# Performance work log

Measured on AMD Instinct MI355X. Metric: run time of the kernel, lower is better.

Reference implementation:

```python
import jax, jax.numpy as jnp
import numpy as np

B, N, E, H = 16, 1024, 1024, 16
D = E // H  # head size = 64

def setup_inputs() -> dict:
    key = jax.random.key(0)
    ks = jax.random.split(key, 5)
    s = 1.0 / np.sqrt(E)
    return {
        "x": jax.random.normal(ks[0], (B, N, E), dtype=jnp.float32),
        "W_qkv": jax.random.normal(ks[1], (E, 3 * E), dtype=jnp.float32) * s,
        "b_qkv": jnp.zeros((3 * E,), dtype=jnp.float32),
        "W_proj": jax.random.normal(ks[2], (E, E), dtype=jnp.float32) * s,
        "b_proj": jnp.zeros((E,), dtype=jnp.float32),
    }

def reference(x, W_qkv, b_qkv, W_proj, b_proj):
    # qkv projection: [B,N,3E]
    qkv = x @ W_qkv + b_qkv
    q, k, v = jnp.split(qkv, 3, axis=-1)
    # b n (h d) -> b h n d
    def split_heads(t):
        return t.reshape(B, N, H, D).transpose(0, 2, 1, 3)
    q, k, v = split_heads(q), split_heads(k), split_heads(v)
    scale = D ** -0.5
    attn = jnp.einsum('bhnd,bhmd->bhnm', q, k) * scale  # [B,H,N,N]
    attn = jax.nn.softmax(attn, axis=-1)
    # dropout p=0 -> identity
    o = jnp.einsum('bhnm,bhmd->bhnd', attn, v)  # [B,H,N,D]
    o = o.transpose(0, 2, 1, 3).reshape(B, N, E)  # b h n d -> b n (h d)
    return o @ W_proj + b_proj
```

## Files before the change

kernel.cpp:

```cpp
#include <hip/hip_runtime.h>
#include <hip/hip_bf16.h>
#include <math.h>

#define BB 16
#define NN 1024
#define EE 1024
#define HH 16
#define DD 64
#define THREE_E 3072
#define M_TOTAL (BB * NN)

typedef __attribute__((ext_vector_type(8))) short bf16x8;
typedef __attribute__((ext_vector_type(4))) short bf16x4;
typedef __attribute__((ext_vector_type(4))) float floatx4;

#define SCALE_Q 0.18033688011112042f

static __device__ __forceinline__ unsigned short f2bf(float f) {
    union { float f; unsigned u; } x; x.f = f;
    unsigned r = x.u + 0x7fffu + ((x.u >> 16) & 1u);
    return (unsigned short)(r >> 16);
}

static __device__ __forceinline__ float fast_exp2(float x) {
#if __has_builtin(__builtin_amdgcn_exp2f)
    return __builtin_amdgcn_exp2f(x);
#else
    float r; __asm__("v_exp_f32 %0, %1" : "=v"(r) : "v"(x)); return r;
#endif
}

static __device__ __forceinline__ bf16x8 pack8v(floatx4 a, floatx4 b) {
    union { bf16x8 v; unsigned u[4]; } r;
    __hip_bfloat162 t;
    t = __float22bfloat162_rn(make_float2(a[0], a[1])); r.u[0] = *(unsigned*)&t;
    t = __float22bfloat162_rn(make_float2(a[2], a[3])); r.u[1] = *(unsigned*)&t;
    t = __float22bfloat162_rn(make_float2(b[0], b[1])); r.u[2] = *(unsigned*)&t;
    t = __float22bfloat162_rn(make_float2(b[2], b[3])); r.u[3] = *(unsigned*)&t;
    return r.v;
}
static __device__ __forceinline__ bf16x8 pack8f(float4 a, float4 b) {
    union { bf16x8 v; unsigned u[4]; } r;
    __hip_bfloat162 t;
    t = __float22bfloat162_rn(make_float2(a.x, a.y)); r.u[0] = *(unsigned*)&t;
    t = __float22bfloat162_rn(make_float2(a.z, a.w)); r.u[1] = *(unsigned*)&t;
    t = __float22bfloat162_rn(make_float2(b.x, b.y)); r.u[2] = *(unsigned*)&t;
    t = __float22bfloat162_rn(make_float2(b.z, b.w)); r.u[3] = *(unsigned*)&t;
    return r.v;
}

#define ASYNC16(gp, lp)                                                \
    __builtin_amdgcn_global_load_lds(                                  \
        (const __attribute__((address_space(1))) void*)(gp),           \
        (__attribute__((address_space(3))) void*)(lp), 16, 0, 0)

#define DRAIN_VMEM() __asm__ __volatile__("s_waitcnt vmcnt(0)" ::: "memory")

__global__ __launch_bounds__(256) void convert_x(
    const float* __restrict__ x, unsigned short* __restrict__ xb)
{
    int i = blockIdx.x * 256 + threadIdx.x;
    const float4* xp = (const float4*)x;
    float4 a = xp[i * 2], b = xp[i * 2 + 1];
    *(bf16x8*)&xb[i * 8] = pack8f(a, b);
}

__global__ __launch_bounds__(256) void wtrans(
    const float* __restrict__ w, unsigned short* __restrict__ wt, int R, int C)
{
    __shared__ float tile[32][33];
    const int t = threadIdx.x;
    const int lr = t >> 5, lc = t & 31;
    const int r0 = blockIdx.y * 32, c0 = blockIdx.x * 32;
    #pragma unroll
    for (int p = 0; p < 4; ++p)
        tile[lr + p * 8][lc] = w[(size_t)(r0 + lr + p * 8) * C + c0 + lc];
    __syncthreads();
    #pragma unroll
    for (int p = 0; p < 4; ++p) {
        int oc = lr + p * 8;
        float v = tile[lc][oc];
        wt[(size_t)(c0 + oc) * R + r0 + lc] = f2bf(v);
    }
}

__global__ __launch_bounds__(256) void gemm_qkv_mfma(
    const unsigned short* __restrict__ xb,
    const unsigned short* __restrict__ wt,
    const float* __restrict__ bias,
    unsigned short* __restrict__ Qo, unsigned short* __restrict__ Ko,
    unsigned short* __restrict__ Vo)
{
    __shared__ __align__(16) unsigned short As[128 * 64];
    __shared__ __align__(16) unsigned short Bs[128 * 64];

    const int t = threadIdx.x;
    const int w = t >> 6, lane = t & 63;
    const int quad = lane >> 4, l15 = lane & 15;
    const int wm = w >> 1, wn = w & 1;
    const int m0 = blockIdx.y * 128;
    const int n0 = blockIdx.x * 128;
    const int srow = lane >> 3;
    const int sch  = lane & 7;
    const int scw  = (sch ^ srow) * 8;
    const int rb   = l15 & 7;

    floatx4 acc[4][4];
    #pragma unroll
    for (int i = 0; i < 4; ++i)
        #pragma unroll
        for (int j = 0; j < 4; ++j) acc[i][j] = (floatx4){0.f, 0.f, 0.f, 0.f};

    const unsigned short* aG = &xb[(size_t)(m0 + w * 8 + srow) * EE + scw];
    const unsigned short* bG = &wt[(size_t)(n0 + w * 8 + srow) * EE + scw];

    for (int kk = 0; kk < EE; kk += 64) {
        #pragma unroll
        for (int p = 0; p < 4; ++p) {
            ASYNC16(aG + kk + (size_t)(p * 32) * EE, &As[(w * 8 + p * 32) * 64]);
            ASYNC16(bG + kk + (size_t)(p * 32) * EE, &Bs[(w * 8 + p * 32) * 64]);
        }
        DRAIN_VMEM();
        __syncthreads();

        #pragma unroll
        for (int s = 0; s < 2; ++s) {
            const int rsw = (((s << 2) | quad) ^ rb) * 8;
            bf16x8 af[4], bf[4];
            #pragma unroll
            for (int i = 0; i < 4; ++i) {
                af[i] = *(const bf16x8*)&As[(wm * 64 + i * 16 + l15) * 64 + rsw];
                bf[i] = *(const bf16x8*)&Bs[(wn * 64 + i * 16 + l15) * 64 + rsw];
            }
            #pragma unroll
            for (int i = 0; i < 4; ++i)
                #pragma unroll
                for (int j = 0; j < 4; ++j)
                    acc[i][j] = __builtin_amdgcn_mfma_f32_16x16x32_bf16(
                        af[i], bf[j], acc[i][j], 0, 0, 0);
        }
        __syncthreads();
    }

    const int mb = m0 + wm * 64;
    const int nb = n0 + wn * 64;
    #pragma unroll
    for (int i = 0; i < 4; ++i) {
        #pragma unroll
        for (int j = 0; j < 4; ++j) {
            int nc = nb + j * 16;
            int which = nc >> 10;
            int e0 = nc & 1023;
            int h  = e0 >> 6;
            int d0 = e0 & 63;
            float bv = bias[nc + l15];
            #pragma unroll
            for (int r = 0; r < 4; ++r) {
                int m = mb + i * 16 + quad * 4 + r;
                int b = m >> 10, n = m & 1023;
                size_t off = ((size_t)(b * HH + h) * NN + n) * DD + d0 + l15;
                float v = acc[i][j][r] + bv;
                if (which == 0)      Qo[off] = f2bf(v * SCALE_Q);
                else if (which == 1) Ko[off] = f2bf(v);
                else                 Vo[off] = f2bf(v);
            }
        }
    }
}

__global__ __launch_bounds__(256) void vtrans(
    const unsigned short* __restrict__ V, unsigned short* __restrict__ Vt)
{
    __shared__ __align__(16) unsigned short tile[64][72];
    const int t  = threadIdx.x;
    const int bh = blockIdx.x;
    const int n0 = blockIdx.y * 64;
    const int r  = t >> 2, c = t & 3;

    const unsigned short* src = &V[((size_t)bh * NN + n0 + r) * DD + c * 16];
    bf16x8 v0 = *(const bf16x8*)&src[0];
    bf16x8 v1 = *(const bf16x8*)&src[8];
    #pragma unroll
    for (int k = 0; k < 8; ++k) tile[c * 16 + k][r]     = v0[k];
    #pragma unroll
    for (int k = 0; k < 8; ++k) tile[c * 16 + 8 + k][r] = v1[k];
    __syncthreads();

    unsigned short* dst = &Vt[((size_t)bh * DD + r) * NN + n0 + c * 16];
    *(bf16x8*)&dst[0] = *(const bf16x8*)&tile[r][c * 16];
    *(bf16x8*)&dst[8] = *(const bf16x8*)&tile[r][c * 16 + 8];
}

__global__ __launch_bounds__(256) void attn_mfma(
    const unsigned short* __restrict__ Q,
    const unsigned short* __restrict__ K,
    const unsigned short* __restrict__ Vt,
    unsigned short* __restrict__ O)
{
    __shared__ __align__(16) unsigned short Ks[64 * 64];
    __shared__ __align__(16) unsigned short Vs[64 * 64];

    const int t    = threadIdx.x;
    const int w    = t >> 6;
    const int quad = (t >> 4) & 3;
    const int l15  = t & 15;
    const int i    = blockIdx.x;
    const int bh   = ((i >> 6) << 3) | (i & 7);
    const int qt   = (i >> 3) & 7;

    const unsigned short* Qg = Q  + (size_t)bh * NN * DD;
    const unsigned short* Kg = K  + (size_t)bh * NN * DD;
    const unsigned short* Vg = Vt + (size_t)bh * DD * NN;

    const int q0 = qt * 128 + w * 32;

    bf16x8 qf[2][2];
    #pragma unroll
    for (int a = 0; a < 2; ++a) {
        qf[a][0] = *(const bf16x8*)&Qg[(size_t)(q0 + a * 16 + l15) * DD + quad * 8];
        qf[a][1] = *(const bf16x8*)&Qg[(size_t)(q0 + a * 16 + l15) * DD + 32 + quad * 8];
    }

    bf16x8 onesA;
    #pragma unroll
    for (int z = 0; z < 8; ++z) onesA[z] = (short)0x3F80;

    floatx4 oa[2][4];
    #pragma unroll
    for (int a = 0; a < 2; ++a)
        #pragma unroll
        for (int jd = 0; jd < 4; ++jd) oa[a][jd] = (floatx4){0.f, 0.f, 0.f, 0.f};
    floatx4 ls[2];
    ls[0] = (floatx4){0.f, 0.f, 0.f, 0.f};
    ls[1] = (floatx4){0.f, 0.f, 0.f, 0.f};

    const int srow = t >> 2;
    const int sc   = t & 3;
    const int swz  = srow & 7;
    const int cbase = ((quad ^ (l15 & 7)) << 3);

    bf16x8 kr0, kr1, vr0, vr1;
    {
        const unsigned short* kg = &Kg[(size_t)srow * DD + sc * 16];
        kr0 = *(const bf16x8*)&kg[0];
        kr1 = *(const bf16x8*)&kg[8];
        const unsigned short* vg = &Vg[(size_t)srow * NN + sc * 16];
        vr0 = *(const bf16x8*)&vg[0];
        vr1 = *(const bf16x8*)&vg[8];
    }

    for (int kt = 0; kt < 16; ++kt) {
        __syncthreads();
        *(bf16x8*)&Ks[srow * 64 + (((2 * sc + 0) ^ swz) << 3)] = kr0;
        *(bf16x8*)&Ks[srow * 64 + (((2 * sc + 1) ^ swz) << 3)] = kr1;
        {
            bf16x4 h[4];
            h[0] = (bf16x4){vr0[0], vr0[1], vr0[2], vr0[3]};
            h[1] = (bf16x4){vr0[4], vr0[5], vr0[6], vr0[7]};
            h[2] = (bf16x4){vr1[0], vr1[1], vr1[2], vr1[3]};
            h[3] = (bf16x4){vr1[4], vr1[5], vr1[6], vr1[7]};
            #pragma unroll
            for (int q = 0; q < 4; ++q) {
                int col = ((((sc >> 1) * 4 + q) ^ swz) << 3) + ((sc & 1) << 2);
                *(bf16x4*)&Vs[srow * 64 + col] = h[q];
            }
        }
        __syncthreads();

        if (kt < 15) {
            const unsigned short* kg =
                &Kg[(size_t)((kt + 1) * 64 + srow) * DD + sc * 16];
            kr0 = *(const bf16x8*)&kg[0];
            kr1 = *(const bf16x8*)&kg[8];
            const unsigned short* vg =
                &Vg[(size_t)srow * NN + (kt + 1) * 64 + sc * 16];
            vr0 = *(const bf16x8*)&vg[0];
            vr1 = *(const bf16x8*)&vg[8];
        }

        floatx4 sa[2][4];
        #pragma unroll
        for (int a = 0; a < 2; ++a)
            #pragma unroll
            for (int tt = 0; tt < 4; ++tt) sa[a][tt] = (floatx4){0.f, 0.f, 0.f, 0.f};
        __builtin_amdgcn_s_setprio(1);
        #pragma unroll
        for (int tt = 0; tt < 4; ++tt) {
            const unsigned short* kb = &Ks[(tt * 16 + l15) * 64];
            bf16x8 kf0 = *(const bf16x8*)&kb[cbase];
            bf16x8 kf1 = *(const bf16x8*)&kb[cbase ^ 32];
            #pragma unroll
            for (int a = 0; a < 2; ++a) {
                sa[a][tt] = __builtin_amdgcn_mfma_f32_16x16x32_bf16(
                    kf0, qf[a][0], sa[a][tt], 0, 0, 0);
                sa[a][tt] = __builtin_amdgcn_mfma_f32_16x16x32_bf16(
                    kf1, qf[a][1], sa[a][tt], 0, 0, 0);
            }
        }
        __builtin_amdgcn_s_setprio(0);

        bf16x8 pf[2][2];
        #pragma unroll
        for (int a = 0; a < 2; ++a) {
            floatx4 pe[4];
            #pragma unroll
            for (int tt = 0; tt < 4; ++tt) {
                #pragma unroll
                for (int r = 0; r < 4; ++r)
                    pe[tt][r] = fast_exp2(sa[a][tt][r]);
            }
            pf[a][0] = pack8v(pe[0], pe[1]);
            pf[a][1] = pack8v(pe[2], pe[3]);
        }

        __builtin_amdgcn_s_setprio(1);
        #pragma unroll
        for (int a = 0; a < 2; ++a) {
            ls[a] = __builtin_amdgcn_mfma_f32_16x16x32_bf16(
                onesA, pf[a][0], ls[a], 0, 0, 0);
            ls[a] = __builtin_amdgcn_mfma_f32_16x16x32_bf16(
                onesA, pf[a][1], ls[a], 0, 0, 0);
        }
        #pragma unroll
        for (int jd = 0; jd < 4; ++jd) {
            const unsigned short* vb = &Vs[(jd * 16 + l15) * 64];
            bf16x8 vf0 = *(const bf16x8*)&vb[cbase];
            bf16x8 vf1 = *(const bf16x8*)&vb[cbase ^ 32];
            #pragma unroll
            for (int a = 0; a < 2; ++a) {
                oa[a][jd] = __builtin_amdgcn_mfma_f32_16x16x32_bf16(
                    vf0, pf[a][0], oa[a][jd], 0, 0, 0);
                oa[a][jd] = __builtin_amdgcn_mfma_f32_16x16x32_bf16(
                    vf1, pf[a][1], oa[a][jd], 0, 0, 0);
            }
        }
        __builtin_amdgcn_s_setprio(0);
    }

    const int b = bh >> 4, h = bh & 15;
    #pragma unroll
    for (int a = 0; a < 2; ++a) {
        float inv = 1.f / ls[a][0];
        int n = q0 + a * 16 + l15;
        size_t base = (size_t)(b * NN + n) * EE + h * DD;
        #pragma unroll
        for (int jd = 0; jd < 4; ++jd) {
            bf16x4 v;
            v[0] = (short)f2bf(oa[a][jd][0] * inv);
            v[1] = (short)f2bf(oa[a][jd][1] * inv);
            v[2] = (short)f2bf(oa[a][jd][2] * inv);
            v[3] = (short)f2bf(oa[a][jd][3] * inv);
            *(bf16x4*)&O[base + jd * 16 + quad * 4] = v;
        }
    }
}

__global__ __launch_bounds__(256) void gemm_proj_mfma(
    const unsigned short* __restrict__ Ob,
    const unsigned short* __restrict__ Bp,
    const float* __restrict__ bias, float* __restrict__ out)
{
    __shared__ __align__(16) unsigned short As[128 * 64];
    __shared__ __align__(16) unsigned short Bs[128 * 64];

    const int t = threadIdx.x;
    const int w = t >> 6, lane = t & 63;
    const int quad = lane >> 4, l15 = lane & 15;
    const int wm = w >> 1, wn = w & 1;
    const int m0 = blockIdx.y * 128;
    const int n0 = blockIdx.x * 128;
    const int srow = lane >> 3;
    const int sch  = lane & 7;
    const int scw  = (sch ^ srow) * 8;
    const int rb   = l15 & 7;

    floatx4 acc[4][4];
    #pragma unroll
    for (int i = 0; i < 4; ++i)
        #pragma unroll
        for (int j = 0; j < 4; ++j) acc[i][j] = (floatx4){0.f, 0.f, 0.f, 0.f};

    const unsigned short* aG = &Ob[(size_t)(m0 + w * 8 + srow) * EE + scw];
    const unsigned short* bG = &Bp[(size_t)(n0 + w * 8 + srow) * EE + scw];

    for (int kk = 0; kk < EE; kk += 64) {
        #pragma unroll
        for (int p = 0; p < 4; ++p) {
            ASYNC16(aG + kk + (size_t)(p * 32) * EE, &As[(w * 8 + p * 32) * 64]);
            ASYNC16(bG + kk + (size_t)(p * 32) * EE, &Bs[(w * 8 + p * 32) * 64]);
        }
        DRAIN_VMEM();
        __syncthreads();

        #pragma unroll
        for (int s = 0; s < 2; ++s) {
            const int rsw = (((s << 2) | quad) ^ rb) * 8;
            bf16x8 af[4], bf[4];
            #pragma unroll
            for (int i = 0; i < 4; ++i) {
                af[i] = *(const bf16x8*)&As[(wm * 64 + i * 16 + l15) * 64 + rsw];
                bf[i] = *(const bf16x8*)&Bs[(wn * 64 + i * 16 + l15) * 64 + rsw];
            }
            #pragma unroll
            for (int i = 0; i < 4; ++i)
                #pragma unroll
                for (int j = 0; j < 4; ++j)
                    acc[i][j] = __builtin_amdgcn_mfma_f32_16x16x32_bf16(
                        af[i], bf[j], acc[i][j], 0, 0, 0);
        }
        __syncthreads();
    }

    const int mb = m0 + wm * 64;
    const int nb = n0 + wn * 64;
    #pragma unroll
    for (int i = 0; i < 4; ++i) {
        #pragma unroll
        for (int j = 0; j < 4; ++j) {
            float bv = bias[nb + j * 16 + l15];
            #pragma unroll
            for (int r = 0; r < 4; ++r) {
                int mrow = mb + i * 16 + quad * 4 + r;
                out[(size_t)mrow * EE + nb + j * 16 + l15] = acc[i][j][r] + bv;
            }
        }
    }
}

extern "C" void kernel_launch(void* const* d_in, const int* in_sizes, int n_in,
                              void* d_out, int out_size, void* d_ws, size_t ws_size,
                              hipStream_t stream) {
    const float* x     = (const float*)d_in[0];
    const float* Wqkv  = (const float*)d_in[1];
    const float* bqkv  = (const float*)d_in[2];
    const float* Wproj = (const float*)d_in[3];
    const float* bproj = (const float*)d_in[4];
    float* out = (float*)d_out;

    const size_t BHND = (size_t)BB * HH * NN * DD;
    unsigned short* Q   = (unsigned short*)d_ws;
    unsigned short* K   = Q   + BHND;
    unsigned short* Vn  = K   + BHND;
    unsigned short* Vt  = Vn  + BHND;
    unsigned short* Ob  = Vt  + BHND;
    unsigned short* xb  = Ob  + BHND;
    unsigned short* Wqt = xb  + BHND;
    unsigned short* Wpt = Wqt + (size_t)THREE_E * EE;

    dim3 blk(256);
    convert_x<<<dim3(M_TOTAL * EE / (256 * 8)), blk, 0, stream>>>(x, xb);
    wtrans<<<dim3(THREE_E / 32, EE / 32), blk, 0, stream>>>(Wqkv, Wqt, EE, THREE_E);
    wtrans<<<dim3(EE / 32, EE / 32), blk, 0, stream>>>(Wproj, Wpt, EE, EE);

    gemm_qkv_mfma<<<dim3(THREE_E / 128, M_TOTAL / 128), blk, 0, stream>>>(
        xb, Wqt, bqkv, Q, K, Vn);
    vtrans<<<dim3(BB * HH, NN / 64), blk, 0, stream>>>(Vn, Vt);
    attn_mfma<<<dim3(BB * HH * NN / 128), blk, 0, stream>>>(Q, K, Vt, Ob);
    gemm_proj_mfma<<<dim3(EE / 128, M_TOTAL / 128), blk, 0, stream>>>(
        Ob, Wpt, bproj, out);
}
```

Before: 404.5 us.

## Double-buffer LDS tiles in QKV and projection GEMMs with async prefetch

Both GEMM kernels now keep two LDS buffers per operand. The tile for step k+1 is issued with global_load_lds while the MFMAs for step k run, which replaces the old load, drain, compute sequence that exposed memory latency on every step. MFMA sections are also wrapped in s_setprio to favour compute issue. This doubles LDS use to 64KB per block, which may lower occupancy. Correctness relies on the single barrier per iteration covering reuse of both buffers.

```diff
diff --git a/kernel.cpp b/kernel.cpp
--- a/kernel.cpp
+++ b/kernel.cpp
@@ -54,8 +54,6 @@
         (const __attribute__((address_space(1))) void*)(gp),           \
         (__attribute__((address_space(3))) void*)(lp), 16, 0, 0)
 
-#define DRAIN_VMEM() __asm__ __volatile__("s_waitcnt vmcnt(0)" ::: "memory")
-
 __global__ __launch_bounds__(256) void convert_x(
     const float* __restrict__ x, unsigned short* __restrict__ xb)
 {
@@ -91,8 +89,8 @@
     unsigned short* __restrict__ Qo, unsigned short* __restrict__ Ko,
     unsigned short* __restrict__ Vo)
 {
-    __shared__ __align__(16) unsigned short As[128 * 64];
-    __shared__ __align__(16) unsigned short Bs[128 * 64];
+    __shared__ __align__(16) unsigned short As[2][128 * 64];
+    __shared__ __align__(16) unsigned short Bs[2][128 * 64];
 
     const int t = threadIdx.x;
     const int w = t >> 6, lane = t & 63;
@@ -114,33 +112,47 @@
     const unsigned short* aG = &xb[(size_t)(m0 + w * 8 + srow) * EE + scw];
     const unsigned short* bG = &wt[(size_t)(n0 + w * 8 + srow) * EE + scw];
 
+#define STAGE_QKV(kk, sl) do {                                              \
+    _Pragma("unroll")                                                       \
+    for (int p = 0; p < 4; ++p) {                                           \
+        ASYNC16(aG + (kk) + (size_t)(p * 32) * EE,                          \
+                &As[sl][(w * 8 + p * 32) * 64]);                            \
+        ASYNC16(bG + (kk) + (size_t)(p * 32) * EE,                          \
+                &Bs[sl][(w * 8 + p * 32) * 64]);                            \
+    } } while (0)
+
+    STAGE_QKV(0, 0);
+    __asm__ __volatile__("s_waitcnt vmcnt(0)" ::: "memory");
+    __builtin_amdgcn_s_barrier();
+
+    #pragma unroll 1
     for (int kk = 0; kk < EE; kk += 64) {
-        #pragma unroll
-        for (int p = 0; p < 4; ++p) {
-            ASYNC16(aG + kk + (size_t)(p * 32) * EE, &As[(w * 8 + p * 32) * 64]);
-            ASYNC16(bG + kk + (size_t)(p * 32) * EE, &Bs[(w * 8 + p * 32) * 64]);
-        }
-        DRAIN_VMEM();
-        __syncthreads();
-
+        const int cur = (kk >> 6) & 1;
+        if (kk + 64 < EE) STAGE_QKV(kk + 64, cur ^ 1);
+        const unsigned short* Asl = As[cur];
+        const unsigned short* Bsl = Bs[cur];
         #pragma unroll
         for (int s = 0; s < 2; ++s) {
             const int rsw = (((s << 2) | quad) ^ rb) * 8;
-            bf16x8 af[4], bf[4];
+            bf16x8 af[4], bfv[4];
             #pragma unroll
             for (int i = 0; i < 4; ++i) {
-                af[i] = *(const bf16x8*)&As[(wm * 64 + i * 16 + l15) * 64 + rsw];
-                bf[i] = *(const bf16x8*)&Bs[(wn * 64 + i * 16 + l15) * 64 + rsw];
-            }
+                af[i]  = *(const bf16x8*)&Asl[(wm * 64 + i * 16 + l15) * 64 + rsw];
+                bfv[i] = *(const bf16x8*)&Bsl[(wn * 64 + i * 16 + l15) * 64 + rsw];
+            }
+            __builtin_amdgcn_s_setprio(1);
             #pragma unroll
             for (int i = 0; i < 4; ++i)
                 #pragma unroll
                 for (int j = 0; j < 4; ++j)
                     acc[i][j] = __builtin_amdgcn_mfma_f32_16x16x32_bf16(
-                        af[i], bf[j], acc[i][j], 0, 0, 0);
-        }
-        __syncthreads();
-    }
+                        af[i], bfv[j], acc[i][j], 0, 0, 0);
+            __builtin_amdgcn_s_setprio(0);
+        }
+        __asm__ __volatile__("s_waitcnt vmcnt(0)" ::: "memory");
+        __builtin_amdgcn_s_barrier();
+    }
+#undef STAGE_QKV
 
     const int mb = m0 + wm * 64;
     const int nb = n0 + wn * 64;
@@ -360,8 +372,8 @@
     const unsigned short* __restrict__ Bp,
     const float* __restrict__ bias, float* __restrict__ out)
 {
-    __shared__ __align__(16) unsigned short As[128 * 64];
-    __shared__ __align__(16) unsigned short Bs[128 * 64];
+    __shared__ __align__(16) unsigned short As[2][128 * 64];
+    __shared__ __align__(16) unsigned short Bs[2][128 * 64];
 
     const int t = threadIdx.x;
     const int w = t >> 6, lane = t & 63;
@@ -383,33 +395,47 @@
     const unsigned short* aG = &Ob[(size_t)(m0 + w * 8 + srow) * EE + scw];
     const unsigned short* bG = &Bp[(size_t)(n0 + w * 8 + srow) * EE + scw];
 
+#define STAGE_PRJ(kk, sl) do {                                              \
+    _Pragma("unroll")                                                       \
+    for (int p = 0; p < 4; ++p) {                                           \
+        ASYNC16(aG + (kk) + (size_t)(p * 32) * EE,                          \
+                &As[sl][(w * 8 + p * 32) * 64]);                            \
+        ASYNC16(bG + (kk) + (size_t)(p * 32) * EE,                          \
+                &Bs[sl][(w * 8 + p * 32) * 64]);                            \
+    } } while (0)
+
+    STAGE_PRJ(0, 0);
+    __asm__ __volatile__("s_waitcnt vmcnt(0)" ::: "memory");
+    __builtin_amdgcn_s_barrier();
+
+    #pragma unroll 1
     for (int kk = 0; kk < EE; kk += 64) {
-        #pragma unroll
-        for (int p = 0; p < 4; ++p) {
-            ASYNC16(aG + kk + (size_t)(p * 32) * EE, &As[(w * 8 + p * 32) * 64]);
-            ASYNC16(bG + kk + (size_t)(p * 32) * EE, &Bs[(w * 8 + p * 32) * 64]);
-        }
-        DRAIN_VMEM();
-        __syncthreads();
-
+        const int cur = (kk >> 6) & 1;
+        if (kk + 64 < EE) STAGE_PRJ(kk + 64, cur ^ 1);
+        const unsigned short* Asl = As[cur];
+        const unsigned short* Bsl = Bs[cur];
         #pragma unroll
         for (int s = 0; s < 2; ++s) {
             const int rsw = (((s << 2) | quad) ^ rb) * 8;
-            bf16x8 af[4], bf[4];
+            bf16x8 af[4], bfv[4];
             #pragma unroll
             for (int i = 0; i < 4; ++i) {
-                af[i] = *(const bf16x8*)&As[(wm * 64 + i * 16 + l15) * 64 + rsw];
-                bf[i] = *(const bf16x8*)&Bs[(wn * 64 + i * 16 + l15) * 64 + rsw];
-            }
+                af[i]  = *(const bf16x8*)&Asl[(wm * 64 + i * 16 + l15) * 64 + rsw];
+                bfv[i] = *(const bf16x8*)&Bsl[(wn * 64 + i * 16 + l15) * 64 + rsw];
+            }
+            __builtin_amdgcn_s_setprio(1);
             #pragma unroll
             for (int i = 0; i < 4; ++i)
                 #pragma unroll
                 for (int j = 0; j < 4; ++j)
                     acc[i][j] = __builtin_amdgcn_mfma_f32_16x16x32_bf16(
-                        af[i], bf[j], acc[i][j], 0, 0, 0);
-        }
-        __syncthreads();
-    }
+                        af[i], bfv[j], acc[i][j], 0, 0, 0);
+            __builtin_amdgcn_s_setprio(0);
+        }
+        __asm__ __volatile__("s_waitcnt vmcnt(0)" ::: "memory");
+        __builtin_amdgcn_s_barrier();
+    }
+#undef STAGE_PRJ
 
     const int mb = m0 + wm * 64;
     const int nb = n0 + wn * 64;
```

Result: no change. 410.4 us (+1.5%).

## Double-buffer K/V tiles in attention and merge prep kernels into one launch

Applied to the files above, without the earlier changes.

Attention now keeps two LDS buffers for K and V. Each iteration writes the next tile into the idle buffer while computing on the current one, which needs one barrier per tile instead of two. The x conversion and the two weight transposes are also merged into a single launch to cut launch overhead. In exchange, LDS use doubles and more registers hold prefetched tiles, which could lower occupancy.

```diff
diff --git a/kernel.cpp b/kernel.cpp
--- a/kernel.cpp
+++ b/kernel.cpp
@@ -56,22 +56,35 @@
 
 #define DRAIN_VMEM() __asm__ __volatile__("s_waitcnt vmcnt(0)" ::: "memory")
 
-__global__ __launch_bounds__(256) void convert_x(
-    const float* __restrict__ x, unsigned short* __restrict__ xb)
-{
-    int i = blockIdx.x * 256 + threadIdx.x;
-    const float4* xp = (const float4*)x;
-    float4 a = xp[i * 2], b = xp[i * 2 + 1];
-    *(bf16x8*)&xb[i * 8] = pack8f(a, b);
-}
-
-__global__ __launch_bounds__(256) void wtrans(
-    const float* __restrict__ w, unsigned short* __restrict__ wt, int R, int C)
+__global__ __launch_bounds__(256) void prep_all(
+    const float* __restrict__ x, unsigned short* __restrict__ xb,
+    const float* __restrict__ Wqkv, unsigned short* __restrict__ Wqt,
+    const float* __restrict__ Wproj, unsigned short* __restrict__ Wpt)
 {
     __shared__ float tile[32][33];
+    const int bid = blockIdx.x;
     const int t = threadIdx.x;
+
+    if (bid < 8192) {
+        int i = bid * 256 + t;
+        const float4* xp = (const float4*)x;
+        float4 a = xp[i * 2], b = xp[i * 2 + 1];
+        *(bf16x8*)&xb[i * 8] = pack8f(a, b);
+        return;
+    }
+
+    const float* w; unsigned short* wt; int R, C, bx, by;
+    if (bid < 8192 + 3072) {
+        int local = bid - 8192;
+        bx = local % 96; by = local / 96;
+        w = Wqkv; wt = Wqt; R = EE; C = THREE_E;
+    } else {
+        int local = bid - 11264;
+        bx = local % 32; by = local / 32;
+        w = Wproj; wt = Wpt; R = EE; C = EE;
+    }
     const int lr = t >> 5, lc = t & 31;
-    const int r0 = blockIdx.y * 32, c0 = blockIdx.x * 32;
+    const int r0 = by * 32, c0 = bx * 32;
     #pragma unroll
     for (int p = 0; p < 4; ++p)
         tile[lr + p * 8][lc] = w[(size_t)(r0 + lr + p * 8) * C + c0 + lc];
@@ -197,8 +210,8 @@
     const unsigned short* __restrict__ Vt,
     unsigned short* __restrict__ O)
 {
-    __shared__ __align__(16) unsigned short Ks[64 * 64];
-    __shared__ __align__(16) unsigned short Vs[64 * 64];
+    __shared__ __align__(16) unsigned short Ks[2][64 * 64];
+    __shared__ __align__(16) unsigned short Vs[2][64 * 64];
 
     const int t    = threadIdx.x;
     const int w    = t >> 6;
@@ -239,103 +252,108 @@
     const int swz  = srow & 7;
     const int cbase = ((quad ^ (l15 & 7)) << 3);
 
-    bf16x8 kr0, kr1, vr0, vr1;
-    {
-        const unsigned short* kg = &Kg[(size_t)srow * DD + sc * 16];
-        kr0 = *(const bf16x8*)&kg[0];
-        kr1 = *(const bf16x8*)&kg[8];
-        const unsigned short* vg = &Vg[(size_t)srow * NN + sc * 16];
-        vr0 = *(const bf16x8*)&vg[0];
-        vr1 = *(const bf16x8*)&vg[8];
-    }
-
-    for (int kt = 0; kt < 16; ++kt) {
-        __syncthreads();
-        *(bf16x8*)&Ks[srow * 64 + (((2 * sc + 0) ^ swz) << 3)] = kr0;
-        *(bf16x8*)&Ks[srow * 64 + (((2 * sc + 1) ^ swz) << 3)] = kr1;
-        {
-            bf16x4 h[4];
-            h[0] = (bf16x4){vr0[0], vr0[1], vr0[2], vr0[3]};
-            h[1] = (bf16x4){vr0[4], vr0[5], vr0[6], vr0[7]};
-            h[2] = (bf16x4){vr1[0], vr1[1], vr1[2], vr1[3]};
-            h[3] = (bf16x4){vr1[4], vr1[5], vr1[6], vr1[7]};
-            #pragma unroll
-            for (int q = 0; q < 4; ++q) {
-                int col = ((((sc >> 1) * 4 + q) ^ swz) << 3) + ((sc & 1) << 2);
-                *(bf16x4*)&Vs[srow * 64 + col] = h[q];
-            }
-        }
-        __syncthreads();
-
-        if (kt < 15) {
-            const unsigned short* kg =
-                &Kg[(size_t)((kt + 1) * 64 + srow) * DD + sc * 16];
-            kr0 = *(const bf16x8*)&kg[0];
-            kr1 = *(const bf16x8*)&kg[8];
-            const unsigned short* vg =
-                &Vg[(size_t)srow * NN + (kt + 1) * 64 + sc * 16];
-            vr0 = *(const bf16x8*)&vg[0];
-            vr1 = *(const bf16x8*)&vg[8];
-        }
-
-        floatx4 sa[2][4];
-        #pragma unroll
-        for (int a = 0; a < 2; ++a)
-            #pragma unroll
-            for (int tt = 0; tt < 4; ++tt) sa[a][tt] = (floatx4){0.f, 0.f, 0.f, 0.f};
-        __builtin_amdgcn_s_setprio(1);
-        #pragma unroll
-        for (int tt = 0; tt < 4; ++tt) {
-            const unsigned short* kb = &Ks[(tt * 16 + l15) * 64];
-            bf16x8 kf0 = *(const bf16x8*)&kb[cbase];
-            bf16x8 kf1 = *(const bf16x8*)&kb[cbase ^ 32];
-            #pragma unroll
-            for (int a = 0; a < 2; ++a) {
-                sa[a][tt] = __builtin_amdgcn_mfma_f32_16x16x32_bf16(
-                    kf0, qf[a][0], sa[a][tt], 0, 0, 0);
-                sa[a][tt] = __builtin_amdgcn_mfma_f32_16x16x32_bf16(
-                    kf1, qf[a][1], sa[a][tt], 0, 0, 0);
-            }
-        }
-        __builtin_amdgcn_s_setprio(0);
-
-        bf16x8 pf[2][2];
-        #pragma unroll
-        for (int a = 0; a < 2; ++a) {
-            floatx4 pe[4];
-            #pragma unroll
-            for (int tt = 0; tt < 4; ++tt) {
-                #pragma unroll
-                for (int r = 0; r < 4; ++r)
-                    pe[tt][r] = fast_exp2(sa[a][tt][r]);
-            }
-            pf[a][0] = pack8v(pe[0], pe[1]);
-            pf[a][1] = pack8v(pe[2], pe[3]);
-        }
-
-        __builtin_amdgcn_s_setprio(1);
-        #pragma unroll
-        for (int a = 0; a < 2; ++a) {
-            ls[a] = __builtin_amdgcn_mfma_f32_16x16x32_bf16(
-                onesA, pf[a][0], ls[a], 0, 0, 0);
-            ls[a] = __builtin_amdgcn_mfma_f32_16x16x32_bf16(
-                onesA, pf[a][1], ls[a], 0, 0, 0);
-        }
-        #pragma unroll
-        for (int jd = 0; jd < 4; ++jd) {
-            const unsigned short* vb = &Vs[(jd * 16 + l15) * 64];
-            bf16x8 vf0 = *(const bf16x8*)&vb[cbase];
-            bf16x8 vf1 = *(const bf16x8*)&vb[cbase ^ 32];
-            #pragma unroll
-            for (int a = 0; a < 2; ++a) {
-                oa[a][jd] = __builtin_amdgcn_mfma_f32_16x16x32_bf16(
-                    vf0, pf[a][0], oa[a][jd], 0, 0, 0);
-                oa[a][jd] = __builtin_amdgcn_mfma_f32_16x16x32_bf16(
-                    vf1, pf[a][1], oa[a][jd], 0, 0, 0);
-            }
-        }
-        __builtin_amdgcn_s_setprio(0);
-    }
+    bf16x8 krA0, krA1, vrA0, vrA1;
+    bf16x8 krB0, krB1, vrB0, vrB1;
+
+#define LOADKV(T, k0, k1, v0, v1) do {                                      \
+    const unsigned short* kg_ = &Kg[(size_t)((T) * 64 + srow) * DD + sc * 16];\
+    k0 = *(const bf16x8*)&kg_[0];                                           \
+    k1 = *(const bf16x8*)&kg_[8];                                           \
+    const unsigned short* vg_ = &Vg[(size_t)srow * NN + (T) * 64 + sc * 16];\
+    v0 = *(const bf16x8*)&vg_[0];                                           \
+    v1 = *(const bf16x8*)&vg_[8]; } while (0)
+
+#define WRITEKV(S, k0, k1, v0, v1) do {                                     \
+    *(bf16x8*)&Ks[S][srow * 64 + (((2 * sc + 0) ^ swz) << 3)] = k0;         \
+    *(bf16x8*)&Ks[S][srow * 64 + (((2 * sc + 1) ^ swz) << 3)] = k1;         \
+    bf16x4 h0_ = (bf16x4){v0[0], v0[1], v0[2], v0[3]};                      \
+    bf16x4 h1_ = (bf16x4){v0[4], v0[5], v0[6], v0[7]};                      \
+    bf16x4 h2_ = (bf16x4){v1[0], v1[1], v1[2], v1[3]};                      \
+    bf16x4 h3_ = (bf16x4){v1[4], v1[5], v1[6], v1[7]};                      \
+    *(bf16x4*)&Vs[S][srow * 64 + (((((sc >> 1) * 4 + 0)) ^ swz) << 3) + ((sc & 1) << 2)] = h0_; \
+    *(bf16x4*)&Vs[S][srow * 64 + (((((sc >> 1) * 4 + 1)) ^ swz) << 3) + ((sc & 1) << 2)] = h1_; \
+    *(bf16x4*)&Vs[S][srow * 64 + (((((sc >> 1) * 4 + 2)) ^ swz) << 3) + ((sc & 1) << 2)] = h2_; \
+    *(bf16x4*)&Vs[S][srow * 64 + (((((sc >> 1) * 4 + 3)) ^ swz) << 3) + ((sc & 1) << 2)] = h3_; \
+    } while (0)
+
+#define COMPUTE(S) do {                                                     \
+    floatx4 sa[2][4];                                                       \
+    _Pragma("unroll")                                                       \
+    for (int a = 0; a < 2; ++a)                                             \
+        _Pragma("unroll")                                                   \
+        for (int tt = 0; tt < 4; ++tt) sa[a][tt] = (floatx4){0.f,0.f,0.f,0.f};\
+    __builtin_amdgcn_s_setprio(1);                                          \
+    _Pragma("unroll")                                                       \
+    for (int tt = 0; tt < 4; ++tt) {                                        \
+        const unsigned short* kb = &Ks[S][(tt * 16 + l15) * 64];            \
+        bf16x8 kf0 = *(const bf16x8*)&kb[cbase];                            \
+        bf16x8 kf1 = *(const bf16x8*)&kb[cbase ^ 32];                       \
+        _Pragma("unroll")                                                   \
+        for (int a = 0; a < 2; ++a) {                                       \
+            sa[a][tt] = __builtin_amdgcn_mfma_f32_16x16x32_bf16(            \
+                kf0, qf[a][0], sa[a][tt], 0, 0, 0);                         \
+            sa[a][tt] = __builtin_amdgcn_mfma_f32_16x16x32_bf16(            \
+                kf1, qf[a][1], sa[a][tt], 0, 0, 0);                         \
+        }                                                                   \
+    }                                                                       \
+    __builtin_amdgcn_s_setprio(0);                                          \
+    bf16x8 pf[2][2];                                                        \
+    _Pragma("unroll")                                                       \
+    for (int a = 0; a < 2; ++a) {                                           \
+        floatx4 pe[4];                                                      \
+        _Pragma("unroll")                                                   \
+        for (int tt = 0; tt < 4; ++tt) {                                    \
+            _Pragma("unroll")                                               \
+            for (int r = 0; r < 4; ++r)                                     \
+                pe[tt][r] = fast_exp2(sa[a][tt][r]);                        \
+        }                                                                   \
+        pf[a][0] = pack8v(pe[0], pe[1]);                                    \
+        pf[a][1] = pack8v(pe[2], pe[3]);                                    \
+    }                                                                       \
+    __builtin_amdgcn_s_setprio(1);                                          \
+    _Pragma("unroll")                                                       \
+    for (int a = 0; a < 2; ++a) {                                           \
+        ls[a] = __builtin_amdgcn_mfma_f32_16x16x32_bf16(                    \
+            onesA, pf[a][0], ls[a], 0, 0, 0);                               \
+        ls[a] = __builtin_amdgcn_mfma_f32_16x16x32_bf16(                    \
+            onesA, pf[a][1], ls[a], 0, 0, 0);                               \
+    }                                                                       \
+    _Pragma("unroll")                                                       \
+    for (int jd = 0; jd < 4; ++jd) {                                        \
+        const unsigned short* vb = &Vs[S][(jd * 16 + l15) * 64];            \
+        bf16x8 vf0 = *(const bf16x8*)&vb[cbase];                            \
+        bf16x8 vf1 = *(const bf16x8*)&vb[cbase ^ 32];                       \
+        _Pragma("unroll")                                                   \
+        for (int a = 0; a < 2; ++a) {                                       \
+            oa[a][jd] = __builtin_amdgcn_mfma_f32_16x16x32_bf16(            \
+                vf0, pf[a][0], oa[a][jd], 0, 0, 0);                         \
+            oa[a][jd] = __builtin_amdgcn_mfma_f32_16x16x32_bf16(            \
+                vf1, pf[a][1], oa[a][jd], 0, 0, 0);                         \
+        }                                                                   \
+    }                                                                       \
+    __builtin_amdgcn_s_setprio(0); } while (0)
+
+    LOADKV(0, krA0, krA1, vrA0, vrA1);
+    WRITEKV(0, krA0, krA1, vrA0, vrA1);
+    LOADKV(1, krB0, krB1, vrB0, vrB1);
+    __syncthreads();
+
+    #pragma unroll 1
+    for (int p = 0; p < 8; ++p) {
+        WRITEKV(1, krB0, krB1, vrB0, vrB1);
+        if (p < 7) LOADKV(2 * p + 2, krA0, krA1, vrA0, vrA1);
+        COMPUTE(0);
+        __syncthreads();
+        if (p < 7) {
+            WRITEKV(0, krA0, krA1, vrA0, vrA1);
+            LOADKV(2 * p + 3, krB0, krB1, vrB0, vrB1);
+        }
+        COMPUTE(1);
+        __syncthreads();
+    }
+#undef LOADKV
+#undef WRITEKV
+#undef COMPUTE
 
     const int b = bh >> 4, h = bh & 15;
     #pragma unroll
@@ -448,9 +466,7 @@
     unsigned short* Wpt = Wqt + (size_t)THREE_E * EE;
 
     dim3 blk(256);
-    convert_x<<<dim3(M_TOTAL * EE / (256 * 8)), blk, 0, stream>>>(x, xb);
-    wtrans<<<dim3(THREE_E / 32, EE / 32), blk, 0, stream>>>(Wqkv, Wqt, EE, THREE_E);
-    wtrans<<<dim3(EE / 32, EE / 32), blk, 0, stream>>>(Wproj, Wpt, EE, EE);
+    prep_all<<<dim3(12288), blk, 0, stream>>>(x, xb, Wqkv, Wqt, Wproj, Wpt);
 
     gemm_qkv_mfma<<<dim3(THREE_E / 128, M_TOTAL / 128), blk, 0, stream>>>(
         xb, Wqt, bqkv, Q, K, Vn);
```

After: 402.4 us. No clear change (-0.5%).
